# Kernel tuning notes

Measured on AMD Instinct MI355X. Metric: run time of the kernel, lower is better.

The kernel has to match this reference:

```python
import jax, jax.numpy as jnp
import numpy as np

D = 1024
H = 4
HD = D // H
B = 256
L = 64
DILATIONS = (1, 4, 8, 16)


def setup_inputs() -> dict:
    key = jax.random.key(0)
    ks = jax.random.split(key, 12)
    s = 1.0 / np.sqrt(D)
    return {
        "x": jax.random.normal(ks[0], (B, D), jnp.float32),
        "hist": jax.random.normal(ks[1], (L, B, D), jnp.float32),
        "Wq": jax.random.normal(ks[2], (D, D), jnp.float32) * s,
        "bq": jnp.zeros((D,), jnp.float32),
        "Wk": jax.random.normal(ks[3], (D, D), jnp.float32) * s,
        "bk": jnp.zeros((D,), jnp.float32),
        "Wv": jax.random.normal(ks[4], (D, D), jnp.float32) * s,
        "bv": jnp.zeros((D,), jnp.float32),
        "Wo": jax.random.normal(ks[5], (D, D), jnp.float32) * s,
        "bo": jnp.zeros((D,), jnp.float32),
        "dil_w": jnp.full((len(DILATIONS),), 1.0 / len(DILATIONS), jnp.float32),
        "gamma": jnp.ones((D,), jnp.float32),
        "beta": jnp.zeros((D,), jnp.float32),
    }


def reference(x, hist, Wq, bq, Wk, bk, Wv, bv, Wo, bo, dil_w, gamma, beta):
    scale = 1.0 / np.sqrt(HD)
    q = (x @ Wq + bq).reshape(B, H, HD)  # (B, H, HD)
    attended = []
    for d in DILATIONS:
        # history frames at stride d, concatenated along dim 0 (faithful to torch.cat)
        frames = hist[::d].reshape(-1, D)              # (T', D), T' = ceil(L/d)*B
        k = (frames @ Wk + bk).reshape(-1, H, HD)      # (T', H, HD)
        v = (frames @ Wv + bv).reshape(-1, H, HD)
        s = jnp.einsum('bhd,thd->bht', q, k) * scale   # (B, H, T')
        a = jax.nn.softmax(s, axis=-1)
        attended.append(jnp.einsum('bht,thd->bhd', a, v).reshape(B, D))
    w = jax.nn.softmax(dil_w, axis=0)
    combined = sum(w[i] * attended[i] for i in range(len(DILATIONS)))
    y = x + combined @ Wo + bo
    mu = jnp.mean(y, axis=-1, keepdims=True)
    var = jnp.var(y, axis=-1, keepdims=True)
    return (y - mu) / jnp.sqrt(var + 1e-5) * gamma + beta
```

## Files before the change

### kernel.cpp

```cpp
#include <hip/hip_runtime.h>


#define DD    1024
#define TALL  16384

typedef _Float16 half8  __attribute__((ext_vector_type(8)));
typedef _Float16 half4v __attribute__((ext_vector_type(4)));
typedef float    floatx4 __attribute__((ext_vector_type(4)));
typedef unsigned int u32;

static const size_t OFF_WOT  = 0;
static const size_t OFF_WV16 = 2097152;
static const size_t OFF_WK16 = 4194304;
static const size_t OFF_WQ16 = 6291456;
static const size_t OFF_XB   = 8388608;
static const size_t OFF_G    = 8912896;
static const size_t OFF_WVOT = 11010048;
static const size_t OFF_WQKT = 19398656;
static const size_t OFF_BVWO = 27787264;
static const size_t OFF_BQK  = 27791360;
static const size_t OFF_PHR  = 27807744;
static const size_t OFF_OPP  = 29904896;
static const size_t OFF_HB   = 38293504;
static const size_t OFF_HT   = 71848960;
static const size_t OFF_S    = 105403392;

__device__ __forceinline__ size_t chunk_off(int g) {
  if (g < 2) return (size_t)g * 4194304;
  if (g < 4) return 19398656 + (size_t)(g - 2) * 4194304;
  if (g < 6) return 29904896 + (size_t)(g - 4) * 4194304;
  return 38293504 + (size_t)(g - 6) * 4194304;
}

__device__ __forceinline__ void gl_lds16(const void* g, void* l) {
  __builtin_amdgcn_global_load_lds((const __attribute__((address_space(1))) u32*)g,
                                   (__attribute__((address_space(3))) u32*)l, 16, 0, 0);
}

__global__ void prep_kernel(const float* __restrict__ Wo, const float* __restrict__ Wv,
                            const float* __restrict__ Wk, const float* __restrict__ Wq,
                            const float* __restrict__ x, const float* __restrict__ hist,
                            _Float16* __restrict__ WoT, _Float16* __restrict__ Wv16,
                            _Float16* __restrict__ Wk16, _Float16* __restrict__ Wq16,
                            _Float16* __restrict__ xb, _Float16* __restrict__ histb,
                            _Float16* __restrict__ histT) {
  int bid = blockIdx.x, tid = threadIdx.x;
  if (bid < 1024) {
    int k0 = (bid & 31) * 32, n0 = (bid >> 5) * 32;
    __shared__ float t32[32][33];
    int tx = tid & 31, ty = tid >> 5;
#pragma unroll
    for (int i = 0; i < 4; i++) {
      int r = ty + i * 8;
      t32[r][tx] = Wo[(size_t)(k0 + r) * DD + n0 + tx];
    }
    __syncthreads();
#pragma unroll
    for (int i = 0; i < 4; i++) {
      int r = ty + i * 8;
      WoT[(size_t)(n0 + r) * DD + k0 + tx] = (_Float16)t32[tx][r];
    }
  } else if (bid < 4352) {
    const float* src; _Float16* dst; size_t i;
    if (bid < 2048)      { src = Wv; dst = Wv16; i = (size_t)(bid - 1024) * 256 + tid; }
    else if (bid < 3072) { src = Wk; dst = Wk16; i = (size_t)(bid - 2048) * 256 + tid; }
    else if (bid < 4096) { src = Wq; dst = Wq16; i = (size_t)(bid - 3072) * 256 + tid; }
    else                 { src = x;  dst = xb;   i = (size_t)(bid - 4096) * 256 + tid; }
    float4 v = ((const float4*)src)[i];
    half4v h = {(_Float16)v.x, (_Float16)v.y, (_Float16)v.z, (_Float16)v.w};
    *(half4v*)(dst + 4 * i) = h;
  } else {
    int tb = bid - 4352;
    int t0 = (tb & 255) * 64, f0 = (tb >> 8) * 64;
    __shared__ _Float16 lt[64][72];
    int r = tid >> 2, c0 = (tid & 3) * 16;
    half8 s0, s1;
#pragma unroll
    for (int i = 0; i < 4; i++) {
      float4 v = *(const float4*)&hist[(size_t)(t0 + r) * 1024 + f0 + c0 + i * 4];
      half4v h = {(_Float16)v.x, (_Float16)v.y, (_Float16)v.z, (_Float16)v.w};
      *(half4v*)&lt[r][c0 + i * 4] = h;
      if (i < 2) { s0[i*4]=h[0]; s0[i*4+1]=h[1]; s0[i*4+2]=h[2]; s0[i*4+3]=h[3]; }
      else { s1[(i-2)*4]=h[0]; s1[(i-2)*4+1]=h[1]; s1[(i-2)*4+2]=h[2]; s1[(i-2)*4+3]=h[3]; }
    }
    *(half8*)&histb[(size_t)(t0 + r) * 1024 + f0 + c0] = s0;
    *(half8*)&histb[(size_t)(t0 + r) * 1024 + f0 + c0 + 8] = s1;
    __syncthreads();
    int fr = tid >> 2, tc0 = (tid & 3) * 16;
    half8 o0, o1;
#pragma unroll
    for (int j = 0; j < 8; j++) { o0[j] = lt[tc0 + j][fr]; o1[j] = lt[tc0 + 8 + j][fr]; }
    *(half8*)&histT[(size_t)(f0 + fr) * TALL + t0 + tc0] = o0;
    *(half8*)&histT[(size_t)(f0 + fr) * TALL + t0 + tc0 + 8] = o1;
  }
}

__device__ __forceinline__ void gemm_core(const _Float16* __restrict__ A, size_t lda,
                                          const _Float16* __restrict__ B, size_t ldb,
                                          int kIters, _Float16* As, _Float16* Bs,
                                          int tid, floatx4 acc[4][4]) {
  int lane = tid & 63, w = tid >> 6;
  int l15 = lane & 15, quad = lane >> 4;
  int wm = (w >> 1) * 64, wn = (w & 1) * 64;
  int swz = ((tid & 3) ^ ((tid >> 3) & 3)) * 8;
  int pch = (quad ^ ((l15 >> 1) & 3)) * 8;
  const char* gA0 = (const char*)(A + (size_t)(tid >> 2) * lda + swz);
  const char* gA1 = (const char*)(A + ((size_t)(tid >> 2) + 64) * lda + swz);
  const char* gB0 = (const char*)(B + (size_t)(tid >> 2) * ldb + swz);
  const char* gB1 = (const char*)(B + ((size_t)(tid >> 2) + 64) * ldb + swz);
  _Float16* lA = As + w * 512;
  _Float16* lB = Bs + w * 512;
#define GC_STAGE(buf, k)                                    \
  do {                                                      \
    size_t off_ = (size_t)(k) * 64;                         \
    gl_lds16(gA0 + off_, lA + (buf) * 4096);                \
    gl_lds16(gA1 + off_, lA + (buf) * 4096 + 2048);         \
    gl_lds16(gB0 + off_, lB + (buf) * 4096);                \
    gl_lds16(gB1 + off_, lB + (buf) * 4096 + 2048);         \
  } while (0)
#define GC_STEP(buf, k)                                                       \
  do {                                                                        \
    if ((k) + 1 < kIters) asm volatile("s_waitcnt vmcnt(4)" ::: "memory");    \
    else                  asm volatile("s_waitcnt vmcnt(0)" ::: "memory");    \
    asm volatile("s_barrier" ::: "memory");                                   \
    const _Float16* Ac_ = As + (buf) * 4096;                                  \
    const _Float16* Bc_ = Bs + (buf) * 4096;                                  \
    half8 a_[4];                                                              \
    _Pragma("unroll")                                                         \
    for (int mi = 0; mi < 4; mi++)                                            \
      a_[mi] = *(const half8*)&Ac_[(wm + mi * 16 + l15) * 32 + pch];          \
    _Pragma("unroll")                                                         \
    for (int ni = 0; ni < 4; ni++) {                                          \
      half8 b8_ = *(const half8*)&Bc_[(wn + ni * 16 + l15) * 32 + pch];       \
      _Pragma("unroll")                                                       \
      for (int mi = 0; mi < 4; mi++)                                          \
        acc[mi][ni] = __builtin_amdgcn_mfma_f32_16x16x32_f16(a_[mi], b8_,     \
                                                             acc[mi][ni], 0, 0, 0); \
    }                                                                         \
    asm volatile("s_waitcnt lgkmcnt(0)" ::: "memory");                        \
    asm volatile("s_barrier" ::: "memory");                                   \
    if ((k) + 2 < kIters) GC_STAGE(buf, (k) + 2);                             \
  } while (0)
  GC_STAGE(0, 0);
  GC_STAGE(1, 1);
  for (int kk = 0; kk < kIters; kk += 2) {
    GC_STEP(0, kk);
    GC_STEP(1, kk + 1);
  }
#undef GC_STEP
#undef GC_STAGE
}

__device__ __forceinline__ void gemm256_core(const _Float16* __restrict__ A, size_t lda,
                                             const _Float16* __restrict__ B, size_t ldb,
                                             int nT, _Float16* As, _Float16* Bs,
                                             int tid, floatx4 acc[8][4]) {
  int lane = tid & 63, w = tid >> 6;
  int l15 = lane & 15, quad = lane >> 4;
  int wr = w >> 2, wc = w & 3;
  int pch = (quad ^ ((l15 >> 1) & 3)) * 8;
  int srow = tid >> 2;
  int schunk = (tid & 3) ^ ((tid >> 3) & 3);
  const char* gA0 = (const char*)(A + (size_t)srow * lda + schunk * 8);
  const char* gA1 = (const char*)(A + (size_t)(srow + 128) * lda + schunk * 8);
  const char* gB0 = (const char*)(B + (size_t)srow * ldb + schunk * 8);
  const char* gB1 = (const char*)(B + (size_t)(srow + 128) * ldb + schunk * 8);
  _Float16* lA = As + w * 512;
  _Float16* lB = Bs + w * 512;
#define ST256(buf, t)                                         \
  do { size_t o_ = (size_t)(t) * 64;                          \
    gl_lds16(gA0 + o_, lA + (buf) * 8192);                    \
    gl_lds16(gA1 + o_, lA + (buf) * 8192 + 4096);             \
    gl_lds16(gB0 + o_, lB + (buf) * 8192);                    \
    gl_lds16(gB1 + o_, lB + (buf) * 8192 + 4096);             \
  } while (0)
  ST256(0, 0);
  ST256(1, 1);
  for (int t = 0; t < nT; ++t) {
    int buf = t & 3;
    if (t + 1 < nT) asm volatile("s_waitcnt vmcnt(4)" ::: "memory");
    else            asm volatile("s_waitcnt vmcnt(0)" ::: "memory");
    asm volatile("s_barrier" ::: "memory");
    if (t + 2 < nT) ST256((t + 2) & 3, t + 2);
    const _Float16* Ac = As + buf * 8192;
    const _Float16* Bc = Bs + buf * 8192;
    half8 b8[4];
#pragma unroll
    for (int ni = 0; ni < 4; ni++)
      b8[ni] = *(const half8*)&Bc[(wc * 64 + ni * 16 + l15) * 32 + pch];
    half8 a8[4];
#pragma unroll
    for (int mi = 0; mi < 4; mi++)
      a8[mi] = *(const half8*)&Ac[(wr * 128 + mi * 16 + l15) * 32 + pch];
    __builtin_amdgcn_s_setprio(1);
#pragma unroll
    for (int mi = 0; mi < 4; mi++)
#pragma unroll
      for (int ni = 0; ni < 4; ni++)
        acc[mi][ni] = __builtin_amdgcn_mfma_f32_16x16x32_f16(a8[mi], b8[ni], acc[mi][ni], 0, 0, 0);
    __builtin_amdgcn_s_setprio(0);
#pragma unroll
    for (int mi = 0; mi < 4; mi++)
      a8[mi] = *(const half8*)&Ac[(wr * 128 + 64 + mi * 16 + l15) * 32 + pch];
    __builtin_amdgcn_s_setprio(1);
#pragma unroll
    for (int mi = 0; mi < 4; mi++)
#pragma unroll
      for (int ni = 0; ni < 4; ni++)
        acc[4 + mi][ni] = __builtin_amdgcn_mfma_f32_16x16x32_f16(a8[mi], b8[ni], acc[4 + mi][ni], 0, 0, 0);
    __builtin_amdgcn_s_setprio(0);
    asm volatile("s_waitcnt lgkmcnt(0)" ::: "memory");
  }
#undef ST256
}

template <bool OUTF32>
__launch_bounds__(256, 3)
__global__ void gemm_f16_kernel(const _Float16* __restrict__ A, size_t lda, size_t aoffz,
                                const _Float16* __restrict__ B, size_t ldb, size_t boffz,
                                int kIters, const float* __restrict__ bias, size_t biasoffz,
                                float scale, void* __restrict__ C, size_t ldc, size_t coffz) {
  __shared__ __align__(16) _Float16 As[8192];
  __shared__ __align__(16) _Float16 Bs[8192];
  int tid = threadIdx.x;
  const _Float16* Ab = A + aoffz * blockIdx.z + (size_t)(blockIdx.y * 128) * lda;
  const _Float16* Bb = B + boffz * blockIdx.z + (size_t)(blockIdx.x * 128) * ldb;
  floatx4 acc[4][4];
  floatx4 zero = {0.f, 0.f, 0.f, 0.f};
#pragma unroll
  for (int a = 0; a < 4; a++)
#pragma unroll
    for (int b = 0; b < 4; b++) acc[a][b] = zero;
  gemm_core(Ab, lda, Bb, ldb, kIters, As, Bs, tid, acc);
  int lane = tid & 63, w = tid >> 6;
  int l15 = lane & 15, quad = lane >> 4;
  int wm = (w >> 1) * 64, wn = (w & 1) * 64;
#pragma unroll
  for (int mi = 0; mi < 4; mi++)
#pragma unroll
    for (int ni = 0; ni < 4; ni++) {
      int colg = blockIdx.x * 128 + wn + ni * 16 + l15;
      float bv = bias ? bias[biasoffz * blockIdx.z + colg] : 0.f;
#pragma unroll
      for (int r = 0; r < 4; r++) {
        int rowg = blockIdx.y * 128 + wm + mi * 16 + quad * 4 + r;
        float v = (acc[mi][ni][r] + bv) * scale;
        size_t idx = coffz * blockIdx.z + (size_t)rowg * ldc + colg;
        if (OUTF32) ((float*)C)[idx] = v;
        else ((_Float16*)C)[idx] = (_Float16)v;
      }
    }
}

__launch_bounds__(256, 3)
__global__ void wpack_kernel(const _Float16* __restrict__ WoT, const _Float16* __restrict__ Wv16,
                             const _Float16* __restrict__ Wk16, const _Float16* __restrict__ Wq16,
                             const float* __restrict__ bv, const float* __restrict__ bq,
                             _Float16* __restrict__ WVOT, _Float16* __restrict__ WQKT,
                             float* __restrict__ bvwo, float* __restrict__ bqk) {
  __shared__ __align__(16) _Float16 As[8192];
  __shared__ __align__(16) _Float16 Bs[8192];
  int bid = blockIdx.x, tid = threadIdx.x;
  if (bid < 512) {
    bool isQK = bid >= 256;
    int g = bid & 255;
    int x = g & 7, y = (g >> 3) & 7, z = g >> 6;
    const _Float16* A = isQK ? Wk16 : WoT;
    const _Float16* B = isQK ? Wq16 : Wv16;
    const _Float16* Ab = A + 256 * z + (size_t)(y * 128) * 1024;
    const _Float16* Bb = B + 256 * z + (size_t)(x * 128) * 1024;
    floatx4 acc[4][4];
    floatx4 zero = {0.f, 0.f, 0.f, 0.f};
#pragma unroll
    for (int a = 0; a < 4; a++)
#pragma unroll
      for (int b = 0; b < 4; b++) acc[a][b] = zero;
    gemm_core(Ab, 1024, Bb, 1024, 8, As, Bs, tid, acc);
    float scale = isQK ? 0.0625f : 1.0f;
    _Float16* C = isQK ? WQKT : WVOT;
    size_t ldc = isQK ? 1024 : 4096;
    size_t zoff = isQK ? (size_t)1048576 * z : (size_t)1024 * z;
    int lane = tid & 63, w = tid >> 6;
    int l15 = lane & 15, quad = lane >> 4;
    int wm = (w >> 1) * 64, wn = (w & 1) * 64;
#pragma unroll
    for (int mi = 0; mi < 4; mi++)
#pragma unroll
      for (int ni = 0; ni < 4; ni++) {
        int col = x * 128 + wn + ni * 16 + l15;
#pragma unroll
        for (int r = 0; r < 4; r++) {
          int row = y * 128 + wm + mi * 16 + quad * 4 + r;
          C[zoff + (size_t)row * ldc + col] = (_Float16)(acc[mi][ni][r] * scale);
        }
      }
  } else if (bid < 516) {
    int j = (bid - 512) * 256 + tid;
    const half8* row = (const half8*)(WoT + (size_t)j * 1024);
    float a = 0.f;
    for (int c = 0; c < 128; c++) {
      half8 w8 = row[c];
#pragma unroll
      for (int e = 0; e < 8; e++) a += bv[c * 8 + e] * (float)w8[e];
    }
    bvwo[j] = a;
  } else {
    int idx = (bid - 516) * 256 + tid;
    int h = idx >> 10, f = idx & 1023;
    const _Float16* row = Wk16 + (size_t)f * 1024 + h * 256;
    float a = 0.f;
    for (int n = 0; n < 256; n++) a += bq[h * 256 + n] * (float)row[n];
    bqk[idx] = a * 0.0625f;
  }
}

__launch_bounds__(512, 2)
__global__ void gemm256_s_kernel(const _Float16* __restrict__ G, const _Float16* __restrict__ histb,
                                 _Float16* __restrict__ S) {
  __shared__ __align__(16) _Float16 As[32768];
  __shared__ __align__(16) _Float16 Bs[32768];
  int bid = blockIdx.x, tid = threadIdx.x;
  int h = bid >> 6, nt = bid & 63;
  const _Float16* Ab = G + (size_t)h * 262144;
  const _Float16* Bb = histb + (size_t)(nt * 256) * 1024;
  floatx4 acc[8][4];
  floatx4 zero = {0.f, 0.f, 0.f, 0.f};
#pragma unroll
  for (int a = 0; a < 8; a++)
#pragma unroll
    for (int b = 0; b < 4; b++) acc[a][b] = zero;
  gemm256_core(Ab, 1024, Bb, 1024, 32, As, Bs, tid, acc);
  int lane = tid & 63, w = tid >> 6;
  int l15 = lane & 15, quad = lane >> 4;
  int wr = w >> 2, wc = w & 3;
#pragma unroll
  for (int mh = 0; mh < 2; mh++)
#pragma unroll
    for (int mi = 0; mi < 4; mi++)
#pragma unroll
      for (int ni = 0; ni < 4; ni++) {
        int col = nt * 256 + wc * 64 + ni * 16 + l15;
#pragma unroll
        for (int r = 0; r < 4; r++) {
          int row = wr * 128 + mh * 64 + mi * 16 + quad * 4 + r;
          S[(size_t)h * 4194304 + (size_t)row * TALL + col] = (_Float16)acc[mh * 4 + mi][ni][r];
        }
      }
}

__global__ void softmax_kernel(_Float16* __restrict__ S, const float* __restrict__ dil_w) {
  int r = blockIdx.x, tid = threadIdx.x;
  _Float16* row = S + (size_t)r * TALL;
  int lane = tid & 63;
  float ef[8][8];
  float es[8];
  __shared__ float Zf[64];
  __shared__ float Zd[4];
  __shared__ float cf[64];
#pragma unroll
  for (int i = 0; i < 8; i++) {
    half8 v = *(const half8*)&row[((size_t)i * 256 + tid) * 8];
    float s = 0.f;
#pragma unroll
    for (int j = 0; j < 8; j++) { float e = __expf((float)v[j]); ef[i][j] = e; s += e; }
#pragma unroll
    for (int off = 1; off <= 16; off <<= 1) s += __shfl_xor(s, off, 64);
    es[i] = s;
  }
  if ((lane & 31) == 0) {
    int half = tid >> 5;
#pragma unroll
    for (int i = 0; i < 8; i++) Zf[i * 8 + half] = es[i];
  }
  __syncthreads();
  if (tid < 4) {
    int step = 1 << (tid + (tid ? 1 : 0));
    float z = 0.f;
    for (int f = 0; f < 64; f += step) z += Zf[f];
    Zd[tid] = z;
  }
  __syncthreads();
  if (tid < 64) {
    float w0 = dil_w[0], w1 = dil_w[1], w2 = dil_w[2], w3 = dil_w[3];
    float wmx = fmaxf(fmaxf(w0, w1), fmaxf(w2, w3));
    float e0 = __expf(w0 - wmx), e1 = __expf(w1 - wmx), e2 = __expf(w2 - wmx), e3 = __expf(w3 - wmx);
    float wsum = e0 + e1 + e2 + e3;
    float c = (e0 / wsum) / Zd[0];
    if ((tid & 3) == 0) c += (e1 / wsum) / Zd[1];
    if ((tid & 7) == 0) c += (e2 / wsum) / Zd[2];
    if ((tid & 15) == 0) c += (e3 / wsum) / Zd[3];
    cf[tid] = c * 256.0f;
  }
  __syncthreads();
#pragma unroll
  for (int i = 0; i < 8; i++) {
    float c = cf[i * 8 + (tid >> 5)];
    half8 o;
#pragma unroll
    for (int j = 0; j < 8; j++) o[j] = (_Float16)(ef[i][j] * c);
    *(half8*)&row[((size_t)i * 256 + tid) * 8] = o;
  }
}

__launch_bounds__(512, 2)
__global__ void gemm256_ph_kernel(const _Float16* __restrict__ P, const _Float16* __restrict__ histT,
                                  char* __restrict__ ws) {
  __shared__ __align__(16) _Float16 As[32768];
  __shared__ __align__(16) _Float16 Bs[32768];
  int bid = blockIdx.x, tid = threadIdx.x;
  int g = bid >> 4, hn = bid & 15;
  int h = hn >> 2, nt = hn & 3;
  int start, nT;
  if (g < 8) { start = g * 37; nT = 37; }
  else       { start = 296 + (g - 8) * 36; nT = 36; }
  const _Float16* Ab = P + (size_t)h * 4194304 + (size_t)start * 32;
  const _Float16* Bb = histT + (size_t)(nt * 256) * TALL + (size_t)start * 32;
  floatx4 acc[8][4];
  floatx4 zero = {0.f, 0.f, 0.f, 0.f};
#pragma unroll
  for (int a = 0; a < 8; a++)
#pragma unroll
    for (int b = 0; b < 4; b++) acc[a][b] = zero;
  gemm256_core(Ab, TALL, Bb, TALL, nT, As, Bs, tid, acc);
  float* chunk = (float*)(ws + chunk_off(g));
  int lane = tid & 63, w = tid >> 6;
  int l15 = lane & 15, quad = lane >> 4;
  int wr = w >> 2, wc = w & 3;
#pragma unroll
  for (int mh = 0; mh < 2; mh++)
#pragma unroll
    for (int mi = 0; mi < 4; mi++)
#pragma unroll
      for (int ni = 0; ni < 4; ni++) {
        int col = h * 1024 + nt * 256 + wc * 64 + ni * 16 + l15;
#pragma unroll
        for (int r = 0; r < 4; r++) {
          int row = wr * 128 + mh * 64 + mi * 16 + quad * 4 + r;
          chunk[(size_t)row * 4096 + col] = acc[mh * 4 + mi][ni][r];
        }
      }
}

__global__ void reduce_ph_kernel(const char* __restrict__ ws, _Float16* __restrict__ PHred) {
  size_t e4 = ((size_t)blockIdx.x * 256 + threadIdx.x) * 4;
  float4 s = {0.f, 0.f, 0.f, 0.f};
#pragma unroll
  for (int g = 0; g < 14; g++) {
    const float* p = (const float*)(ws + chunk_off(g));
    float4 v = *(const float4*)&p[e4];
    s.x += v.x; s.y += v.y; s.z += v.z; s.w += v.w;
  }
  half4v o = {(_Float16)s.x, (_Float16)s.y, (_Float16)s.z, (_Float16)s.w};
  *(half4v*)&PHred[e4] = o;
}

__global__ void ln_kernel(const float* __restrict__ x, const float* __restrict__ part2,
                          const float* __restrict__ bo, const float* __restrict__ bvwo,
                          const float* __restrict__ gamma, const float* __restrict__ beta,
                          float* __restrict__ out) {
  int b = blockIdx.x, t = threadIdx.x;
  __shared__ float red[8];
  float y[4];
  float sum = 0.f, sq = 0.f;
#pragma unroll
  for (int i = 0; i < 4; i++) {
    int j = t + i * 256;
    float v = x[(size_t)b * 1024 + j] + bo[j] + bvwo[j];
#pragma unroll
    for (int z = 0; z < 8; z++) v += part2[(size_t)z * 262144 + (size_t)b * 1024 + j];
    y[i] = v;
    sum += v;
    sq += v * v;
  }
#pragma unroll
  for (int off = 1; off < 64; off <<= 1) {
    sum += __shfl_xor(sum, off, 64);
    sq += __shfl_xor(sq, off, 64);
  }
  int w = t >> 6, lane = t & 63;
  if (lane == 0) { red[w] = sum; red[4 + w] = sq; }
  __syncthreads();
  sum = red[0] + red[1] + red[2] + red[3];
  sq = red[4] + red[5] + red[6] + red[7];
  float mu = sum * (1.f / 1024.f);
  float var = sq * (1.f / 1024.f) - mu * mu;
  float inv = rsqrtf(var + 1e-5f);
#pragma unroll
  for (int i = 0; i < 4; i++) {
    int j = t + i * 256;
    out[(size_t)b * 1024 + j] = (y[i] - mu) * inv * gamma[j] + beta[j];
  }
}

extern "C" void kernel_launch(void* const* d_in, const int* in_sizes, int n_in,
                              void* d_out, int out_size, void* d_ws, size_t ws_size,
                              hipStream_t stream) {
  const float* x     = (const float*)d_in[0];
  const float* hist  = (const float*)d_in[1];
  const float* Wq    = (const float*)d_in[2];
  const float* bq    = (const float*)d_in[3];
  const float* Wk    = (const float*)d_in[4];
  const float* Wv    = (const float*)d_in[6];
  const float* bv    = (const float*)d_in[7];
  const float* Wo    = (const float*)d_in[8];
  const float* bo    = (const float*)d_in[9];
  const float* dil_w = (const float*)d_in[10];
  const float* gamma = (const float*)d_in[11];
  const float* beta  = (const float*)d_in[12];
  char* ws = (char*)d_ws;

  _Float16* WoT   = (_Float16*)(ws + OFF_WOT);
  _Float16* Wv16  = (_Float16*)(ws + OFF_WV16);
  _Float16* Wk16  = (_Float16*)(ws + OFF_WK16);
  _Float16* Wq16  = (_Float16*)(ws + OFF_WQ16);
  _Float16* xb    = (_Float16*)(ws + OFF_XB);
  _Float16* G     = (_Float16*)(ws + OFF_G);
  _Float16* WVOT  = (_Float16*)(ws + OFF_WVOT);
  _Float16* WQKT  = (_Float16*)(ws + OFF_WQKT);
  float* bvwo     = (float*)(ws + OFF_BVWO);
  float* bqk      = (float*)(ws + OFF_BQK);
  _Float16* PHred = (_Float16*)(ws + OFF_PHR);
  float* oppart   = (float*)(ws + OFF_OPP);
  _Float16* histb = (_Float16*)(ws + OFF_HB);
  _Float16* histT = (_Float16*)(ws + OFF_HT);
  _Float16* Sb    = (_Float16*)(ws + OFF_S);

  prep_kernel<<<dim3(8448), 256, 0, stream>>>(Wo, Wv, Wk, Wq, x, hist,
                                              WoT, Wv16, Wk16, Wq16, xb, histb, histT);
  wpack_kernel<<<dim3(532), 256, 0, stream>>>(WoT, Wv16, Wk16, Wq16, bv, bq,
                                              WVOT, WQKT, bvwo, bqk);
  gemm_f16_kernel<false><<<dim3(8, 2, 4), 256, 0, stream>>>(
      xb, 1024, 0, WQKT, 1024, 1048576, 32, bqk, 1024, 1.0f, (void*)G, 1024, 262144);
  gemm256_s_kernel<<<dim3(256), 512, 0, stream>>>(G, histb, Sb);
  softmax_kernel<<<dim3(1024), 256, 0, stream>>>(Sb, dil_w);
  gemm256_ph_kernel<<<dim3(224), 512, 0, stream>>>(Sb, histT, ws);
  reduce_ph_kernel<<<dim3(1024), 256, 0, stream>>>(ws, PHred);
  gemm_f16_kernel<true><<<dim3(8, 2, 8), 256, 0, stream>>>(
      PHred, 4096, 512, WVOT, 4096, 512, 16, nullptr, 0, 1.0f / 256.0f,
      (void*)oppart, 1024, 262144);
  ln_kernel<<<dim3(256), 256, 0, stream>>>(x, oppart, bo, bvwo, gamma, beta, (float*)d_out);
}
```

Measured before the change: 342.3 us.

## Deepen GEMM prefetch, rebalance PH split-K to 16 chunks with fp16 partials

The shared 256-tile GEMM core now keeps three tiles in flight instead of two, using the fourth LDS buffer with adjusted waitcnt levels. The PH GEMM moves from 14 uneven K-splits to 16 equal splits of 32 tiles, so 256 blocks fill the device. Blocks are mapped so that each XCD handles whole K-groups. Partial sums are stored as fp16 instead of fp32, which halves workspace traffic for the GEMM writeback and the reduction, at the cost of some precision in the partial accumulations.

```diff
diff --git a/kernel.cpp b/kernel.cpp
--- a/kernel.cpp
+++ b/kernel.cpp
@@ -25,11 +25,11 @@
 static const size_t OFF_HT   = 71848960;
 static const size_t OFF_S    = 105403392;
 
-__device__ __forceinline__ size_t chunk_off(int g) {
-  if (g < 2) return (size_t)g * 4194304;
-  if (g < 4) return 19398656 + (size_t)(g - 2) * 4194304;
-  if (g < 6) return 29904896 + (size_t)(g - 4) * 4194304;
-  return 38293504 + (size_t)(g - 6) * 4194304;
+__device__ __forceinline__ size_t chunk16_off(int g) {
+  if (g < 4)  return (size_t)g * 2097152;
+  if (g < 8)  return 19398656 + (size_t)(g - 4) * 2097152;
+  if (g < 12) return 29904896 + (size_t)(g - 8) * 2097152;
+  return 38293504 + (size_t)(g - 12) * 2097152;
 }
 
 __device__ __forceinline__ void gl_lds16(const void* g, void* l) {
@@ -175,13 +175,15 @@
     gl_lds16(gB1 + o_, lB + (buf) * 8192 + 4096);             \
   } while (0)
   ST256(0, 0);
-  ST256(1, 1);
+  if (nT > 1) ST256(1, 1);
+  if (nT > 2) ST256(2, 2);
   for (int t = 0; t < nT; ++t) {
     int buf = t & 3;
-    if (t + 1 < nT) asm volatile("s_waitcnt vmcnt(4)" ::: "memory");
-    else            asm volatile("s_waitcnt vmcnt(0)" ::: "memory");
+    if (t + 2 < nT)      asm volatile("s_waitcnt vmcnt(8)" ::: "memory");
+    else if (t + 1 < nT) asm volatile("s_waitcnt vmcnt(4)" ::: "memory");
+    else                 asm volatile("s_waitcnt vmcnt(0)" ::: "memory");
     asm volatile("s_barrier" ::: "memory");
-    if (t + 2 < nT) ST256((t + 2) & 3, t + 2);
+    if (t + 3 < nT) ST256((t + 3) & 3, t + 3);
     const _Float16* Ac = As + buf * 8192;
     const _Float16* Bc = Bs + buf * 8192;
     half8 b8[4];
@@ -408,21 +410,20 @@
   __shared__ __align__(16) _Float16 As[32768];
   __shared__ __align__(16) _Float16 Bs[32768];
   int bid = blockIdx.x, tid = threadIdx.x;
-  int g = bid >> 4, hn = bid & 15;
-  int h = hn >> 2, nt = hn & 3;
-  int start, nT;
-  if (g < 8) { start = g * 37; nT = 37; }
-  else       { start = 296 + (g - 8) * 36; nT = 36; }
-  const _Float16* Ab = P + (size_t)h * 4194304 + (size_t)start * 32;
-  const _Float16* Bb = histT + (size_t)(nt * 256) * TALL + (size_t)start * 32;
+  int xcd = bid & 7, slot = bid >> 3;
+  int g = xcd + 8 * (slot >> 4);
+  int member = slot & 15;
+  int h = member >> 2, nt = member & 3;
+  const _Float16* Ab = P + (size_t)h * 4194304 + (size_t)g * 1024;
+  const _Float16* Bb = histT + (size_t)(nt * 256) * TALL + (size_t)g * 1024;
   floatx4 acc[8][4];
   floatx4 zero = {0.f, 0.f, 0.f, 0.f};
 #pragma unroll
   for (int a = 0; a < 8; a++)
 #pragma unroll
     for (int b = 0; b < 4; b++) acc[a][b] = zero;
-  gemm256_core(Ab, TALL, Bb, TALL, nT, As, Bs, tid, acc);
-  float* chunk = (float*)(ws + chunk_off(g));
+  gemm256_core(Ab, TALL, Bb, TALL, 32, As, Bs, tid, acc);
+  _Float16* chunk = (_Float16*)(ws + chunk16_off(g));
   int lane = tid & 63, w = tid >> 6;
   int l15 = lane & 15, quad = lane >> 4;
   int wr = w >> 2, wc = w & 3;
@@ -436,22 +437,25 @@
 #pragma unroll
         for (int r = 0; r < 4; r++) {
           int row = wr * 128 + mh * 64 + mi * 16 + quad * 4 + r;
-          chunk[(size_t)row * 4096 + col] = acc[mh * 4 + mi][ni][r];
+          chunk[(size_t)row * 4096 + col] = (_Float16)acc[mh * 4 + mi][ni][r];
         }
       }
 }
 
 __global__ void reduce_ph_kernel(const char* __restrict__ ws, _Float16* __restrict__ PHred) {
-  size_t e4 = ((size_t)blockIdx.x * 256 + threadIdx.x) * 4;
-  float4 s = {0.f, 0.f, 0.f, 0.f};
-#pragma unroll
-  for (int g = 0; g < 14; g++) {
-    const float* p = (const float*)(ws + chunk_off(g));
-    float4 v = *(const float4*)&p[e4];
-    s.x += v.x; s.y += v.y; s.z += v.z; s.w += v.w;
-  }
-  half4v o = {(_Float16)s.x, (_Float16)s.y, (_Float16)s.z, (_Float16)s.w};
-  *(half4v*)&PHred[e4] = o;
+  size_t e8 = ((size_t)blockIdx.x * 256 + threadIdx.x) * 8;
+  float s[8] = {0.f, 0.f, 0.f, 0.f, 0.f, 0.f, 0.f, 0.f};
+#pragma unroll
+  for (int g = 0; g < 16; g++) {
+    const _Float16* p = (const _Float16*)(ws + chunk16_off(g));
+    half8 v = *(const half8*)&p[e8];
+#pragma unroll
+    for (int j = 0; j < 8; j++) s[j] += (float)v[j];
+  }
+  half8 o;
+#pragma unroll
+  for (int j = 0; j < 8; j++) o[j] = (_Float16)s[j];
+  *(half8*)&PHred[e8] = o;
 }
 
 __global__ void ln_kernel(const float* __restrict__ x, const float* __restrict__ part2,
@@ -533,8 +537,8 @@
       xb, 1024, 0, WQKT, 1024, 1048576, 32, bqk, 1024, 1.0f, (void*)G, 1024, 262144);
   gemm256_s_kernel<<<dim3(256), 512, 0, stream>>>(G, histb, Sb);
   softmax_kernel<<<dim3(1024), 256, 0, stream>>>(Sb, dil_w);
-  gemm256_ph_kernel<<<dim3(224), 512, 0, stream>>>(Sb, histT, ws);
-  reduce_ph_kernel<<<dim3(1024), 256, 0, stream>>>(ws, PHred);
+  gemm256_ph_kernel<<<dim3(256), 512, 0, stream>>>(Sb, histT, ws);
+  reduce_ph_kernel<<<dim3(512), 256, 0, stream>>>(ws, PHred);
   gemm_f16_kernel<true><<<dim3(8, 2, 8), 256, 0, stream>>>(
       PHred, 4096, 512, WVOT, 4096, 512, 16, nullptr, 0, 1.0f / 256.0f,
       (void*)oppart, 1024, 262144);
```

Result: faster. 327.4 us (-4.3%).
